# Performance work log

Measured on AMD Instinct MI355X. Metric: run time of the kernel, lower is better.

The kernel has to match this reference:

```python
import jax, jax.numpy as jnp
import numpy as np

NUM_HEADS = 16
NUM_KV_HEADS = 4
HEAD_DIM = 128
ROPE_BASE = 10000.0


def _apply_rope(x):
    # x: [B, H, S, D], interleaved RoPE: x1 = x[..., ::2], x2 = x[..., 1::2]
    B, H, S, D = x.shape
    inv_freq = 1.0 / (ROPE_BASE ** (jnp.arange(0, D, 2, dtype=jnp.float32) / D))  # [D/2]
    t = jnp.arange(S, dtype=jnp.float32)
    freqs = t[:, None] * inv_freq[None, :]          # [S, D/2]
    cos = jnp.cos(freqs)[None, None]                # [1,1,S,D/2]
    sin = jnp.sin(freqs)[None, None]
    xr = x.reshape(B, H, S, D // 2, 2)
    x1, x2 = xr[..., 0], xr[..., 1]
    r1 = x1 * cos - x2 * sin
    r2 = x1 * sin + x2 * cos
    return jnp.stack([r1, r2], axis=-1).reshape(B, H, S, D)


def setup_inputs() -> dict:
    key = jax.random.key(0)
    ks = jax.random.split(key, 5)
    H = NUM_HEADS * HEAD_DIM          # 2048
    KV = NUM_KV_HEADS * HEAD_DIM      # 512
    std = 0.02
    return {
        "hidden_states": jax.random.normal(ks[0], (1, 4096, H), dtype=jnp.float32),
        "wq": jax.random.normal(ks[1], (H, H), dtype=jnp.float32) * std,
        "wk": jax.random.normal(ks[2], (H, KV), dtype=jnp.float32) * std,
        "wv": jax.random.normal(ks[3], (H, KV), dtype=jnp.float32) * std,
        "wo": jax.random.normal(ks[4], (H, H), dtype=jnp.float32) * std,
    }


def reference(hidden_states, wq, wk, wv, wo):
    B, S, H = hidden_states.shape
    nh, nkv, hd = NUM_HEADS, NUM_KV_HEADS, HEAD_DIM
    scale = 1.0 / np.sqrt(hd)

    q = (hidden_states @ wq).reshape(B, S, nh, hd).transpose(0, 2, 1, 3)   # [B,nh,S,hd]
    k = (hidden_states @ wk).reshape(B, S, nkv, hd).transpose(0, 2, 1, 3)  # [B,nkv,S,hd]
    v = (hidden_states @ wv).reshape(B, S, nkv, hd).transpose(0, 2, 1, 3)

    q = _apply_rope(q)
    k = _apply_rope(k)

    rep = nh // nkv
    k = jnp.repeat(k, rep, axis=1)  # GQA head repetition -> [B,nh,S,hd]
    v = jnp.repeat(v, rep, axis=1)

    scores = jnp.einsum("bhqd,bhkd->bhqk", q, k) * scale
    causal = jnp.tril(jnp.ones((S, S), dtype=bool))
    scores = jnp.where(causal[None, None], scores, jnp.float32(-1e30))
    probs = jax.nn.softmax(scores, axis=-1)
    attn = jnp.einsum("bhqk,bhkd->bhqd", probs, v)      # [B,nh,S,hd]
    attn = attn.transpose(0, 2, 1, 3).reshape(B, S, H)
    return attn @ wo
```

## Files before the change

kernel.cpp:

```cpp
#include <hip/hip_runtime.h>

typedef unsigned short u16;
typedef unsigned int u32;
typedef __bf16 bf16x8 __attribute__((ext_vector_type(8)));
typedef float f32x4 __attribute__((ext_vector_type(4)));
typedef float f32x16 __attribute__((ext_vector_type(16)));
typedef int v2i __attribute__((ext_vector_type(2)));

#define S_LEN 4096
#define HDIM 2048
#define KVDIM 512
#define N_HEADS 16
#define HEAD_D 128

__device__ __forceinline__ u16 f2bf(float f) {
  u32 u = __float_as_uint(f);
  u32 r = (u + 0x7FFFu + ((u >> 16) & 1u)) >> 16;
  return (u16)r;
}
__device__ __forceinline__ float bf2f(u16 h) {
  return __uint_as_float(((u32)h) << 16);
}
__device__ __forceinline__ float exp2_fast(float x) {
  float r;
  asm("v_exp_f32 %0, %1" : "=v"(r) : "v"(x));
  return r;
}
__device__ __forceinline__ u32 cvt_pk_bf16(float lo, float hi) {
  u32 r;
  asm("v_cvt_pk_bf16_f32 %0, %1, %2" : "=v"(r) : "v"(lo), "v"(hi));
  return r;
}
__device__ __forceinline__ void gload16(const u16* g, const u16* l) {
  __builtin_amdgcn_global_load_lds(
      (const __attribute__((address_space(1))) void*)g,
      (__attribute__((address_space(3))) void*)l, 16, 0, 0);
}

__global__ void k_prep(const float* __restrict__ in, u16* __restrict__ out,
                       float* __restrict__ cosT, float* __restrict__ sinT) {
  int b = blockIdx.x;
  int tid = threadIdx.x;
  if (b < 4096) {
    int i = b * 256 + tid;
    const float4* p = reinterpret_cast<const float4*>(in) + (size_t)i * 2;
    float4 a = p[0], c = p[1];
    u32 o0 = (u32)f2bf(a.x) | ((u32)f2bf(a.y) << 16);
    u32 o1 = (u32)f2bf(a.z) | ((u32)f2bf(a.w) << 16);
    u32 o2 = (u32)f2bf(c.x) | ((u32)f2bf(c.y) << 16);
    u32 o3 = (u32)f2bf(c.z) | ((u32)f2bf(c.w) << 16);
    reinterpret_cast<uint4*>(out)[i] = make_uint4(o0, o1, o2, o3);
  } else {
    int i = (b - 4096) * 256 + tid;
    int pos = i >> 6, f = i & 63;
    float inv = expf(-0.1439115683121279f * (float)f);
    float ang = (float)pos * inv;
    float s, c;
    sincosf(ang, &s, &c);
    cosT[i] = c;
    sinT[i] = s;
  }
}

__global__ void k_transpose_all(const float* __restrict__ wq, const float* __restrict__ wk,
                                const float* __restrict__ wv, const float* __restrict__ wo,
                                u16* __restrict__ WqT, u16* __restrict__ WkT,
                                u16* __restrict__ WvT, u16* __restrict__ WoT) {
  __shared__ float t[32][33];
  int b = blockIdx.x;
  const float* W;
  u16* Wt;
  int Kd, Nd, bx, by;
  if (b < 4096) {
    W = wq; Wt = WqT; Kd = HDIM; Nd = HDIM; bx = b & 63; by = b >> 6;
  } else if (b < 5120) {
    int r = b - 4096; W = wk; Wt = WkT; Kd = HDIM; Nd = KVDIM; bx = r & 15; by = r >> 4;
  } else if (b < 6144) {
    int r = b - 5120; W = wv; Wt = WvT; Kd = HDIM; Nd = KVDIM; bx = r & 15; by = r >> 4;
  } else {
    int r = b - 6144; W = wo; Wt = WoT; Kd = HDIM; Nd = HDIM; bx = r & 63; by = r >> 6;
  }
  int tx = threadIdx.x & 31, ty = threadIdx.x >> 5;
  int n = bx * 32 + tx;
  for (int j = ty; j < 32; j += 8)
    t[j][tx] = W[(size_t)(by * 32 + j) * Nd + n];
  __syncthreads();
  int k = by * 32 + tx;
  for (int j = ty; j < 32; j += 8)
    Wt[(size_t)(bx * 32 + j) * Kd + k] = f2bf(t[tx][j]);
}

__global__ void k_rope_all(u16* __restrict__ Qb, u16* __restrict__ Kb,
                           const float* __restrict__ cosT, const float* __restrict__ sinT) {
  int b = blockIdx.x;
  u16* X;
  int width, i;
  if (b < 4096) { X = Qb; width = HDIM; i = b * 256 + threadIdx.x; }
  else { X = Kb; width = KVDIM; i = (b - 4096) * 256 + threadIdx.x; }
  size_t idx = (size_t)i * 8;
  int row = (int)(idx / width);
  int col = (int)(idx - (size_t)row * width);
  int fi = (col & 127) >> 1;
  float4 c4 = *reinterpret_cast<const float4*>(&cosT[(row << 6) + fi]);
  float4 s4 = *reinterpret_cast<const float4*>(&sinT[(row << 6) + fi]);
  uint4 v = *reinterpret_cast<const uint4*>(&X[idx]);
  float cc[4] = {c4.x, c4.y, c4.z, c4.w};
  float ss[4] = {s4.x, s4.y, s4.z, s4.w};
  u32 w_[4] = {v.x, v.y, v.z, v.w};
  u32 r_[4];
#pragma unroll
  for (int p = 0; p < 4; ++p) {
    float x1 = bf2f((u16)(w_[p] & 0xffff));
    float x2 = bf2f((u16)(w_[p] >> 16));
    float r1 = x1 * cc[p] - x2 * ss[p];
    float r2 = x1 * ss[p] + x2 * cc[p];
    r_[p] = (u32)f2bf(r1) | ((u32)f2bf(r2) << 16);
  }
  *reinterpret_cast<uint4*>(&X[idx]) = make_uint4(r_[0], r_[1], r_[2], r_[3]);
}

__global__ __launch_bounds__(256) void k_gemm_qkv(
    const u16* __restrict__ A, const u16* __restrict__ WqT, const u16* __restrict__ WkT,
    const u16* __restrict__ WvT, u16* __restrict__ Qb, u16* __restrict__ Kb,
    u16* __restrict__ VTb) {
  const int Kd = HDIM, M = S_LEN;
  __shared__ __align__(16) u16 As[128 * 32];
  __shared__ __align__(16) u16 Bs[128 * 32];
  const int p = blockIdx.x;
  const int bmg = p & 7, r = p >> 3;
  const int bm = (bmg * 4 + (r & 3)) * 128;
  const int by = r >> 2;
  const u16* Bt;
  int bn, N, mode;
  if (by < 16) { Bt = WqT; bn = by * 128; N = HDIM; mode = 0; }
  else if (by < 20) { Bt = WkT; bn = (by - 16) * 128; N = KVDIM; mode = 1; }
  else { Bt = WvT; bn = (by - 20) * 128; N = KVDIM; mode = 2; }
  const int tid = threadIdx.x;
  const int lane = tid & 63;
  const int wid = tid >> 6;
  const int wr = (wid >> 1) * 64, wc = (wid & 1) * 64;
  const int lr = lane & 15, lhi = lane >> 4;
  const int srow = lane >> 2;
  const int skc = (lane & 3) * 8;
  f32x4 acc[4][4] = {};
  for (int k0 = 0; k0 < Kd; k0 += 32) {
#pragma unroll
    for (int it = 0; it < 2; ++it) {
      int rowbase = (it * 4 + wid) * 16;
      gload16(&A[(size_t)(bm + rowbase + srow) * Kd + k0 + skc], &As[rowbase * 32]);
      gload16(&Bt[(size_t)(bn + rowbase + srow) * Kd + k0 + skc], &Bs[rowbase * 32]);
    }
    __syncthreads();
    bf16x8 af[4], bfr[4];
#pragma unroll
    for (int m = 0; m < 4; ++m)
      af[m] = *reinterpret_cast<const bf16x8*>(&As[(wr + m * 16 + lr) * 32 + lhi * 8]);
#pragma unroll
    for (int n = 0; n < 4; ++n)
      bfr[n] = *reinterpret_cast<const bf16x8*>(&Bs[(wc + n * 16 + lr) * 32 + lhi * 8]);
#pragma unroll
    for (int m = 0; m < 4; ++m)
#pragma unroll
      for (int n = 0; n < 4; ++n)
        acc[m][n] = __builtin_amdgcn_mfma_f32_16x16x32_bf16(af[m], bfr[n], acc[m][n], 0, 0, 0);
    __syncthreads();
  }
#pragma unroll
  for (int m = 0; m < 4; ++m) {
    int grow0 = bm + wr + m * 16 + lhi * 4;
#pragma unroll
    for (int n = 0; n < 4; ++n) {
      int gcol = bn + wc + n * 16 + lr;
      if (mode == 2) {
        ushort4 pk;
        pk.x = f2bf(acc[m][n][0]);
        pk.y = f2bf(acc[m][n][1]);
        pk.z = f2bf(acc[m][n][2]);
        pk.w = f2bf(acc[m][n][3]);
        *reinterpret_cast<ushort4*>(&VTb[(size_t)gcol * M + grow0]) = pk;
      } else {
        u16* outp = (mode == 0) ? Qb : Kb;
#pragma unroll
        for (int r2 = 0; r2 < 4; ++r2)
          outp[(size_t)(grow0 + r2) * N + gcol] = f2bf(acc[m][n][r2]);
      }
    }
  }
}

__global__ __launch_bounds__(256) void k_gemm_bt(
    const u16* __restrict__ A, const u16* __restrict__ Bt, float* __restrict__ Cout,
    int M, int N, int Kd) {
  __shared__ __align__(16) u16 As[128 * 32];
  __shared__ __align__(16) u16 Bs[128 * 32];
  const int p = blockIdx.x;
  const int bmg = p & 7, r = p >> 3;
  const int bm = (bmg * 4 + (r & 3)) * 128;
  const int bn = (r >> 2) * 128;
  const int tid = threadIdx.x;
  const int lane = tid & 63;
  const int wid = tid >> 6;
  const int wr = (wid >> 1) * 64, wc = (wid & 1) * 64;
  const int lr = lane & 15, lhi = lane >> 4;
  const int srow = lane >> 2;
  const int skc = (lane & 3) * 8;
  f32x4 acc[4][4] = {};
  for (int k0 = 0; k0 < Kd; k0 += 32) {
#pragma unroll
    for (int it = 0; it < 2; ++it) {
      int rowbase = (it * 4 + wid) * 16;
      gload16(&A[(size_t)(bm + rowbase + srow) * Kd + k0 + skc], &As[rowbase * 32]);
      gload16(&Bt[(size_t)(bn + rowbase + srow) * Kd + k0 + skc], &Bs[rowbase * 32]);
    }
    __syncthreads();
    bf16x8 af[4], bfr[4];
#pragma unroll
    for (int m = 0; m < 4; ++m)
      af[m] = *reinterpret_cast<const bf16x8*>(&As[(wr + m * 16 + lr) * 32 + lhi * 8]);
#pragma unroll
    for (int n = 0; n < 4; ++n)
      bfr[n] = *reinterpret_cast<const bf16x8*>(&Bs[(wc + n * 16 + lr) * 32 + lhi * 8]);
#pragma unroll
    for (int m = 0; m < 4; ++m)
#pragma unroll
      for (int n = 0; n < 4; ++n)
        acc[m][n] = __builtin_amdgcn_mfma_f32_16x16x32_bf16(af[m], bfr[n], acc[m][n], 0, 0, 0);
    __syncthreads();
  }
#pragma unroll
  for (int m = 0; m < 4; ++m) {
    int grow0 = bm + wr + m * 16 + lhi * 4;
#pragma unroll
    for (int n = 0; n < 4; ++n) {
      int gcol = bn + wc + n * 16 + lr;
#pragma unroll
      for (int r2 = 0; r2 < 4; ++r2)
        Cout[(size_t)(grow0 + r2) * N + gcol] = acc[m][n][r2];
    }
  }
}

__global__ __launch_bounds__(256, 2) void k_attn(
    const u16* __restrict__ Q, const u16* __restrict__ K, const u16* __restrict__ VT,
    u16* __restrict__ PO0, u16* __restrict__ PO1, float2* __restrict__ ML) {
  __shared__ __align__(16) u16 Ks[64 * 128];
  __shared__ __align__(16) u16 Vs[128 * 64];
  int i = blockIdx.x;
  const int kvhalf = i >> 9;
  int jj = i & 511;
  int qt, h;
  if (jj < 256) { qt = 16 + (jj & 15); h = jj >> 4; }
  else { int j2 = jj - 256; qt = 15 - (j2 & 15); h = j2 >> 4; }
  const int kvh = h >> 2;
  const int tid = threadIdx.x, lane = tid & 63, wid = tid >> 6;
  const int l31 = lane & 31, hi = lane >> 5;
  const int qw = qt * 128 + wid * 32;
  const int qglob = qw + l31;
  const float CE = 0.12751743f;
  const float THR = 62.74f;

  const u16* qptr = &Q[(size_t)qglob * HDIM + h * HEAD_D];
  bf16x8 qf[8];
#pragma unroll
  for (int ks = 0; ks < 8; ++ks)
    qf[ks] = *reinterpret_cast<const bf16x8*>(&qptr[ks * 16 + hi * 8]);

  f32x16 o_[4] = {};
  float m_ = -3e38f, l_ = 0.f;
  char* KsB = (char*)Ks;
  char* VsB = (char*)Vs;

  const int j0 = kvhalf * (qt + 1);
  const int j1 = j0 + qt + 1;
  for (int j = j0; j < j1; ++j) {
    const int kb = j << 6;
    __syncthreads();
#pragma unroll
    for (int it = 0; it < 4; ++it) {
      int s = it * 256 + tid;
      int kv = s >> 4, c16 = s & 15;
      int db = kv * 256 + c16 * 16;
      db ^= ((db >> 8) & 7) << 4;
      *reinterpret_cast<uint4*>(KsB + db) = *reinterpret_cast<const uint4*>(
          &K[(size_t)(kb + kv) * KVDIM + kvh * HEAD_D + c16 * 8]);
    }
#pragma unroll
    for (int it = 0; it < 4; ++it) {
      int s = it * 256 + tid;
      int d = s >> 3, k16 = s & 7;
      int db = d * 128 + k16 * 16;
      db ^= ((db >> 7) & 7) << 4;
      *reinterpret_cast<uint4*>(VsB + db) = *reinterpret_cast<const uint4*>(
          &VT[(size_t)(kvh * HEAD_D + d) * S_LEN + kb + k16 * 8]);
    }
    __syncthreads();

    if (kb <= qw + 31) {
      f32x16 s0 = {}, s1 = {};
#pragma unroll
      for (int ks = 0; ks < 8; ++ks) {
        int db0 = l31 * 256 + ks * 32 + hi * 16;
        db0 ^= ((db0 >> 8) & 7) << 4;
        int db1 = (32 + l31) * 256 + ks * 32 + hi * 16;
        db1 ^= ((db1 >> 8) & 7) << 4;
        bf16x8 k0 = *reinterpret_cast<const bf16x8*>(KsB + db0);
        bf16x8 k1 = *reinterpret_cast<const bf16x8*>(KsB + db1);
        s0 = __builtin_amdgcn_mfma_f32_32x32x16_bf16(k0, qf[ks], s0, 0, 0, 0);
        s1 = __builtin_amdgcn_mfma_f32_32x32x16_bf16(k1, qf[ks], s1, 0, 0, 0);
      }
      if (kb + 63 > qw) {
#pragma unroll
        for (int r = 0; r < 16; ++r) {
          int kvr = kb + (r & 3) + 8 * (r >> 2) + 4 * hi;
          if (kvr > qglob) s0[r] = -1e30f;
          if (kvr + 32 > qglob) s1[r] = -1e30f;
        }
      }
      float pm = fmaxf(s0[0], s1[0]);
#pragma unroll
      for (int r = 1; r < 16; ++r) pm = fmaxf(pm, fmaxf(s0[r], s1[r]));
      pm = fmaxf(pm, __shfl_xor(pm, 32));
      if (!__all(pm <= m_ + THR)) {
        float mnew = fmaxf(m_, pm);
        float fac = exp2_fast((m_ - mnew) * CE);
        m_ = mnew;
        l_ *= fac;
#pragma unroll
        for (int dt = 0; dt < 4; ++dt)
#pragma unroll
          for (int r = 0; r < 16; ++r) o_[dt][r] *= fac;
      }
      const float mc = m_ * CE;
      float rs = 0.f;
#pragma unroll
      for (int r = 0; r < 16; ++r) {
        s0[r] = exp2_fast(__builtin_fmaf(s0[r], CE, -mc));
        s1[r] = exp2_fast(__builtin_fmaf(s1[r], CE, -mc));
        rs += s0[r] + s1[r];
      }
      rs += __shfl_xor(rs, 32);
      l_ += rs;
#pragma unroll
      for (int kvt = 0; kvt < 2; ++kvt) {
        u32 xw[8], yw[8];
#pragma unroll
        for (int g = 0; g < 8; ++g) {
          float plo = kvt ? s1[2 * g] : s0[2 * g];
          float phi = kvt ? s1[2 * g + 1] : s0[2 * g + 1];
          u32 pw = cvt_pk_bf16(plo, phi);
          v2i sw = __builtin_amdgcn_permlane32_swap((int)pw, (int)pw, false, false);
          xw[g] = (u32)sw[0];
          yw[g] = (u32)sw[1];
        }
#pragma unroll
        for (int ksl = 0; ksl < 2; ++ksl) {
          int b = ksl * 4;
          u32 f0 = hi ? xw[b + 2] : xw[b + 0];
          u32 f1 = hi ? xw[b + 3] : xw[b + 1];
          u32 f2 = hi ? yw[b + 2] : yw[b + 0];
          u32 f3 = hi ? yw[b + 3] : yw[b + 1];
          uint4 fr = make_uint4(f0, f1, f2, f3);
          bf16x8 pf = *reinterpret_cast<bf16x8*>(&fr);
          const int kvstep = kvt * 2 + ksl;
#pragma unroll
          for (int dt = 0; dt < 4; ++dt) {
            int db = (dt * 32 + l31) * 128 + kvstep * 32 + hi * 16;
            db ^= ((db >> 7) & 7) << 4;
            bf16x8 vf = *reinterpret_cast<const bf16x8*>(VsB + db);
            o_[dt] = __builtin_amdgcn_mfma_f32_32x32x16_bf16(vf, pf, o_[dt], 0, 0, 0);
          }
        }
      }
    }
  }
  const float inv_l = (l_ > 0.f) ? (1.0f / l_) : 0.f;
  u16* PO = kvhalf ? PO1 : PO0;
  u16* optr = &PO[(size_t)qglob * HDIM + h * HEAD_D];
#pragma unroll
  for (int dt = 0; dt < 4; ++dt)
#pragma unroll
    for (int g = 0; g < 4; ++g) {
      ushort4 pk;
      pk.x = f2bf(o_[dt][4 * g + 0] * inv_l);
      pk.y = f2bf(o_[dt][4 * g + 1] * inv_l);
      pk.z = f2bf(o_[dt][4 * g + 2] * inv_l);
      pk.w = f2bf(o_[dt][4 * g + 3] * inv_l);
      *reinterpret_cast<ushort4*>(&optr[dt * 32 + g * 8 + hi * 4]) = pk;
    }
  if (hi == 0)
    ML[(size_t)kvhalf * N_HEADS * S_LEN + (size_t)h * S_LEN + qglob] =
        make_float2(m_, l_);
}

__global__ void k_combine(const u16* __restrict__ PO0, const u16* __restrict__ PO1,
                          const float2* __restrict__ ML, u16* __restrict__ Out) {
  int i = blockIdx.x * 256 + threadIdx.x;
  int d8 = (i & 15) * 8;
  int qh = i >> 4;
  int h = qh & 15, q = qh >> 4;
  const float CE = 0.12751743f;
  float2 ml1 = ML[(size_t)h * S_LEN + q];
  float2 ml2 = ML[(size_t)N_HEADS * S_LEN + (size_t)h * S_LEN + q];
  float m = fmaxf(ml1.x, ml2.x);
  float w1 = ml1.y * exp2_fast((ml1.x - m) * CE);
  float w2 = ml2.y * exp2_fast((ml2.x - m) * CE);
  float inv = 1.0f / (w1 + w2);
  w1 *= inv;
  w2 *= inv;
  size_t base = (size_t)q * HDIM + h * HEAD_D + d8;
  uint4 a = *reinterpret_cast<const uint4*>(&PO0[base]);
  uint4 b = *reinterpret_cast<const uint4*>(&PO1[base]);
  u32 aw[4] = {a.x, a.y, a.z, a.w}, bw[4] = {b.x, b.y, b.z, b.w};
  u32 ow[4];
#pragma unroll
  for (int p = 0; p < 4; ++p) {
    float lo = w1 * bf2f((u16)(aw[p] & 0xffff)) + w2 * bf2f((u16)(bw[p] & 0xffff));
    float hi2 = w1 * bf2f((u16)(aw[p] >> 16)) + w2 * bf2f((u16)(bw[p] >> 16));
    ow[p] = (u32)f2bf(lo) | ((u32)f2bf(hi2) << 16);
  }
  *reinterpret_cast<uint4*>(&Out[base]) = make_uint4(ow[0], ow[1], ow[2], ow[3]);
}

extern "C" void kernel_launch(void* const* d_in, const int* in_sizes, int n_in,
                              void* d_out, int out_size, void* d_ws, size_t ws_size,
                              hipStream_t stream) {
  const float* hs = (const float*)d_in[0];
  const float* wq = (const float*)d_in[1];
  const float* wk = (const float*)d_in[2];
  const float* wv = (const float*)d_in[3];
  const float* wo = (const float*)d_in[4];

  char* ws = (char*)d_ws;
  size_t off = 0;
  auto alloc = [&](size_t bytes) {
    void* p = ws + off;
    off += (bytes + 255) & ~(size_t)255;
    return p;
  };
  u16* Xb = (u16*)alloc((size_t)S_LEN * HDIM * 2);
  u16* WqT = (u16*)alloc((size_t)HDIM * HDIM * 2);
  u16* WkT = (u16*)alloc((size_t)KVDIM * HDIM * 2);
  u16* WvT = (u16*)alloc((size_t)KVDIM * HDIM * 2);
  u16* WoT = (u16*)alloc((size_t)HDIM * HDIM * 2);
  u16* Qb = (u16*)alloc((size_t)S_LEN * HDIM * 2);
  u16* Kb = (u16*)alloc((size_t)S_LEN * KVDIM * 2);
  u16* VTb = (u16*)alloc((size_t)KVDIM * S_LEN * 2);
  u16* Ab = (u16*)alloc((size_t)S_LEN * HDIM * 2);
  float* cosT = (float*)alloc((size_t)S_LEN * 64 * 4);
  float* sinT = (float*)alloc((size_t)S_LEN * 64 * 4);
  if (off > ws_size) return;

  u16* PO0 = Ab;
  u16* PO1 = Xb;
  float2* ML = (float2*)WqT;

  k_prep<<<dim3(5120), dim3(256), 0, stream>>>(hs, Xb, cosT, sinT);
  k_transpose_all<<<dim3(10240), dim3(256), 0, stream>>>(wq, wk, wv, wo, WqT, WkT, WvT, WoT);
  k_gemm_qkv<<<dim3(768), dim3(256), 0, stream>>>(Xb, WqT, WkT, WvT, Qb, Kb, VTb);
  k_rope_all<<<dim3(5120), dim3(256), 0, stream>>>(Qb, Kb, cosT, sinT);
  k_attn<<<dim3(1024), dim3(256), 0, stream>>>(Qb, Kb, VTb, PO0, PO1, ML);
  k_combine<<<dim3(4096), dim3(256), 0, stream>>>(PO0, PO1, ML, Ab);
  k_gemm_bt<<<dim3(512), dim3(256), 0, stream>>>(Ab, WoT, (float*)d_out, S_LEN, HDIM, HDIM);
}
```

Before: 277.4 us.

## Fuse RoPE into QKV epilogue, combine into output GEMM, merge prep kernels

The input conversion, cos/sin table generation and weight transposes now share one launch instead of two. RoPE is applied in the QKV GEMM epilogue: each lane swaps its value with its neighbour via __shfl_xor and combines it with cos/sin read from the tables. The split-KV combine is folded into the output GEMM's A-tile load, so the pass that read the two partial outputs and wrote a merged buffer goes away. The cost is that the output GEMM now does synchronous global loads plus combine arithmetic, replacing the async global_load_lds, and repeats that work for every N tile.

```diff
diff --git a/kernel.cpp b/kernel.cpp
--- a/kernel.cpp
+++ b/kernel.cpp
@@ -37,8 +37,13 @@
       (__attribute__((address_space(3))) void*)l, 16, 0, 0);
 }
 
-__global__ void k_prep(const float* __restrict__ in, u16* __restrict__ out,
-                       float* __restrict__ cosT, float* __restrict__ sinT) {
+__global__ void k_prep_all(const float* __restrict__ in, u16* __restrict__ out,
+                           float* __restrict__ cosT, float* __restrict__ sinT,
+                           const float* __restrict__ wq, const float* __restrict__ wk,
+                           const float* __restrict__ wv, const float* __restrict__ wo,
+                           u16* __restrict__ WqT, u16* __restrict__ WkT,
+                           u16* __restrict__ WvT, u16* __restrict__ WoT) {
+  __shared__ float t[32][33];
   int b = blockIdx.x;
   int tid = threadIdx.x;
   if (b < 4096) {
@@ -50,7 +55,9 @@
     u32 o2 = (u32)f2bf(c.x) | ((u32)f2bf(c.y) << 16);
     u32 o3 = (u32)f2bf(c.z) | ((u32)f2bf(c.w) << 16);
     reinterpret_cast<uint4*>(out)[i] = make_uint4(o0, o1, o2, o3);
-  } else {
+    return;
+  }
+  if (b < 5120) {
     int i = (b - 4096) * 256 + tid;
     int pos = i >> 6, f = i & 63;
     float inv = expf(-0.1439115683121279f * (float)f);
@@ -59,28 +66,22 @@
     sincosf(ang, &s, &c);
     cosT[i] = c;
     sinT[i] = s;
-  }
-}
-
-__global__ void k_transpose_all(const float* __restrict__ wq, const float* __restrict__ wk,
-                                const float* __restrict__ wv, const float* __restrict__ wo,
-                                u16* __restrict__ WqT, u16* __restrict__ WkT,
-                                u16* __restrict__ WvT, u16* __restrict__ WoT) {
-  __shared__ float t[32][33];
-  int b = blockIdx.x;
+    return;
+  }
+  int bb = b - 5120;
   const float* W;
   u16* Wt;
   int Kd, Nd, bx, by;
-  if (b < 4096) {
-    W = wq; Wt = WqT; Kd = HDIM; Nd = HDIM; bx = b & 63; by = b >> 6;
-  } else if (b < 5120) {
-    int r = b - 4096; W = wk; Wt = WkT; Kd = HDIM; Nd = KVDIM; bx = r & 15; by = r >> 4;
-  } else if (b < 6144) {
-    int r = b - 5120; W = wv; Wt = WvT; Kd = HDIM; Nd = KVDIM; bx = r & 15; by = r >> 4;
+  if (bb < 4096) {
+    W = wq; Wt = WqT; Kd = HDIM; Nd = HDIM; bx = bb & 63; by = bb >> 6;
+  } else if (bb < 5120) {
+    int r = bb - 4096; W = wk; Wt = WkT; Kd = HDIM; Nd = KVDIM; bx = r & 15; by = r >> 4;
+  } else if (bb < 6144) {
+    int r = bb - 5120; W = wv; Wt = WvT; Kd = HDIM; Nd = KVDIM; bx = r & 15; by = r >> 4;
   } else {
-    int r = b - 6144; W = wo; Wt = WoT; Kd = HDIM; Nd = HDIM; bx = r & 63; by = r >> 6;
-  }
-  int tx = threadIdx.x & 31, ty = threadIdx.x >> 5;
+    int r = bb - 6144; W = wo; Wt = WoT; Kd = HDIM; Nd = HDIM; bx = r & 63; by = r >> 6;
+  }
+  int tx = tid & 31, ty = tid >> 5;
   int n = bx * 32 + tx;
   for (int j = ty; j < 32; j += 8)
     t[j][tx] = W[(size_t)(by * 32 + j) * Nd + n];
@@ -90,38 +91,10 @@
     Wt[(size_t)(bx * 32 + j) * Kd + k] = f2bf(t[tx][j]);
 }
 
-__global__ void k_rope_all(u16* __restrict__ Qb, u16* __restrict__ Kb,
-                           const float* __restrict__ cosT, const float* __restrict__ sinT) {
-  int b = blockIdx.x;
-  u16* X;
-  int width, i;
-  if (b < 4096) { X = Qb; width = HDIM; i = b * 256 + threadIdx.x; }
-  else { X = Kb; width = KVDIM; i = (b - 4096) * 256 + threadIdx.x; }
-  size_t idx = (size_t)i * 8;
-  int row = (int)(idx / width);
-  int col = (int)(idx - (size_t)row * width);
-  int fi = (col & 127) >> 1;
-  float4 c4 = *reinterpret_cast<const float4*>(&cosT[(row << 6) + fi]);
-  float4 s4 = *reinterpret_cast<const float4*>(&sinT[(row << 6) + fi]);
-  uint4 v = *reinterpret_cast<const uint4*>(&X[idx]);
-  float cc[4] = {c4.x, c4.y, c4.z, c4.w};
-  float ss[4] = {s4.x, s4.y, s4.z, s4.w};
-  u32 w_[4] = {v.x, v.y, v.z, v.w};
-  u32 r_[4];
-#pragma unroll
-  for (int p = 0; p < 4; ++p) {
-    float x1 = bf2f((u16)(w_[p] & 0xffff));
-    float x2 = bf2f((u16)(w_[p] >> 16));
-    float r1 = x1 * cc[p] - x2 * ss[p];
-    float r2 = x1 * ss[p] + x2 * cc[p];
-    r_[p] = (u32)f2bf(r1) | ((u32)f2bf(r2) << 16);
-  }
-  *reinterpret_cast<uint4*>(&X[idx]) = make_uint4(r_[0], r_[1], r_[2], r_[3]);
-}
-
 __global__ __launch_bounds__(256) void k_gemm_qkv(
     const u16* __restrict__ A, const u16* __restrict__ WqT, const u16* __restrict__ WkT,
-    const u16* __restrict__ WvT, u16* __restrict__ Qb, u16* __restrict__ Kb,
+    const u16* __restrict__ WvT, const float* __restrict__ cosT,
+    const float* __restrict__ sinT, u16* __restrict__ Qb, u16* __restrict__ Kb,
     u16* __restrict__ VTb) {
   const int Kd = HDIM, M = S_LEN;
   __shared__ __align__(16) u16 As[128 * 32];
@@ -165,6 +138,7 @@
         acc[m][n] = __builtin_amdgcn_mfma_f32_16x16x32_bf16(af[m], bfr[n], acc[m][n], 0, 0, 0);
     __syncthreads();
   }
+  const float odd_sign = (lr & 1) ? 1.0f : -1.0f;
 #pragma unroll
   for (int m = 0; m < 4; ++m) {
     int grow0 = bm + wr + m * 16 + lhi * 4;
@@ -180,17 +154,27 @@
         *reinterpret_cast<ushort4*>(&VTb[(size_t)gcol * M + grow0]) = pk;
       } else {
         u16* outp = (mode == 0) ? Qb : Kb;
-#pragma unroll
-        for (int r2 = 0; r2 < 4; ++r2)
-          outp[(size_t)(grow0 + r2) * N + gcol] = f2bf(acc[m][n][r2]);
+        const int fi = (gcol & 127) >> 1;
+#pragma unroll
+        for (int r2 = 0; r2 < 4; ++r2) {
+          float v = acc[m][n][r2];
+          float pv = __shfl_xor(v, 1);
+          int pos = grow0 + r2;
+          float c = cosT[(pos << 6) + fi];
+          float s = sinT[(pos << 6) + fi];
+          float res = __builtin_fmaf(pv, odd_sign * s, v * c);
+          outp[(size_t)pos * N + gcol] = f2bf(res);
+        }
       }
     }
   }
 }
 
 __global__ __launch_bounds__(256) void k_gemm_bt(
-    const u16* __restrict__ A, const u16* __restrict__ Bt, float* __restrict__ Cout,
-    int M, int N, int Kd) {
+    const u16* __restrict__ PO0, const u16* __restrict__ PO1,
+    const float2* __restrict__ ML, const u16* __restrict__ Bt,
+    float* __restrict__ Cout) {
+  const int M = S_LEN, N = HDIM, Kd = HDIM;
   __shared__ __align__(16) u16 As[128 * 32];
   __shared__ __align__(16) u16 Bs[128 * 32];
   const int p = blockIdx.x;
@@ -204,12 +188,35 @@
   const int lr = lane & 15, lhi = lane >> 4;
   const int srow = lane >> 2;
   const int skc = (lane & 3) * 8;
+  const float CE = 0.12751743f;
   f32x4 acc[4][4] = {};
   for (int k0 = 0; k0 < Kd; k0 += 32) {
+    const int hh = (k0 + skc) >> 7;
 #pragma unroll
     for (int it = 0; it < 2; ++it) {
       int rowbase = (it * 4 + wid) * 16;
-      gload16(&A[(size_t)(bm + rowbase + srow) * Kd + k0 + skc], &As[rowbase * 32]);
+      int row = bm + rowbase + srow;
+      float2 ml1 = ML[(size_t)hh * S_LEN + row];
+      float2 ml2 = ML[(size_t)N_HEADS * S_LEN + (size_t)hh * S_LEN + row];
+      float mm = fmaxf(ml1.x, ml2.x);
+      float w1 = ml1.y * exp2_fast((ml1.x - mm) * CE);
+      float w2 = ml2.y * exp2_fast((ml2.x - mm) * CE);
+      float inv = 1.0f / (w1 + w2);
+      w1 *= inv;
+      w2 *= inv;
+      size_t gbase = (size_t)row * Kd + k0 + skc;
+      uint4 a = *reinterpret_cast<const uint4*>(&PO0[gbase]);
+      uint4 b = *reinterpret_cast<const uint4*>(&PO1[gbase]);
+      u32 aw[4] = {a.x, a.y, a.z, a.w}, bw[4] = {b.x, b.y, b.z, b.w};
+      u32 ow[4];
+#pragma unroll
+      for (int q = 0; q < 4; ++q) {
+        float lo = w1 * bf2f((u16)(aw[q] & 0xffff)) + w2 * bf2f((u16)(bw[q] & 0xffff));
+        float hi2 = w1 * bf2f((u16)(aw[q] >> 16)) + w2 * bf2f((u16)(bw[q] >> 16));
+        ow[q] = cvt_pk_bf16(lo, hi2);
+      }
+      *reinterpret_cast<uint4*>(&As[(rowbase + srow) * 32 + skc]) =
+          make_uint4(ow[0], ow[1], ow[2], ow[3]);
       gload16(&Bt[(size_t)(bn + rowbase + srow) * Kd + k0 + skc], &Bs[rowbase * 32]);
     }
     __syncthreads();
@@ -390,35 +397,6 @@
   if (hi == 0)
     ML[(size_t)kvhalf * N_HEADS * S_LEN + (size_t)h * S_LEN + qglob] =
         make_float2(m_, l_);
-}
-
-__global__ void k_combine(const u16* __restrict__ PO0, const u16* __restrict__ PO1,
-                          const float2* __restrict__ ML, u16* __restrict__ Out) {
-  int i = blockIdx.x * 256 + threadIdx.x;
-  int d8 = (i & 15) * 8;
-  int qh = i >> 4;
-  int h = qh & 15, q = qh >> 4;
-  const float CE = 0.12751743f;
-  float2 ml1 = ML[(size_t)h * S_LEN + q];
-  float2 ml2 = ML[(size_t)N_HEADS * S_LEN + (size_t)h * S_LEN + q];
-  float m = fmaxf(ml1.x, ml2.x);
-  float w1 = ml1.y * exp2_fast((ml1.x - m) * CE);
-  float w2 = ml2.y * exp2_fast((ml2.x - m) * CE);
-  float inv = 1.0f / (w1 + w2);
-  w1 *= inv;
-  w2 *= inv;
-  size_t base = (size_t)q * HDIM + h * HEAD_D + d8;
-  uint4 a = *reinterpret_cast<const uint4*>(&PO0[base]);
-  uint4 b = *reinterpret_cast<const uint4*>(&PO1[base]);
-  u32 aw[4] = {a.x, a.y, a.z, a.w}, bw[4] = {b.x, b.y, b.z, b.w};
-  u32 ow[4];
-#pragma unroll
-  for (int p = 0; p < 4; ++p) {
-    float lo = w1 * bf2f((u16)(aw[p] & 0xffff)) + w2 * bf2f((u16)(bw[p] & 0xffff));
-    float hi2 = w1 * bf2f((u16)(aw[p] >> 16)) + w2 * bf2f((u16)(bw[p] >> 16));
-    ow[p] = (u32)f2bf(lo) | ((u32)f2bf(hi2) << 16);
-  }
-  *reinterpret_cast<uint4*>(&Out[base]) = make_uint4(ow[0], ow[1], ow[2], ow[3]);
 }
 
 extern "C" void kernel_launch(void* const* d_in, const int* in_sizes, int n_in,
@@ -454,11 +432,9 @@
   u16* PO1 = Xb;
   float2* ML = (float2*)WqT;
 
-  k_prep<<<dim3(5120), dim3(256), 0, stream>>>(hs, Xb, cosT, sinT);
-  k_transpose_all<<<dim3(10240), dim3(256), 0, stream>>>(wq, wk, wv, wo, WqT, WkT, WvT, WoT);
-  k_gemm_qkv<<<dim3(768), dim3(256), 0, stream>>>(Xb, WqT, WkT, WvT, Qb, Kb, VTb);
-  k_rope_all<<<dim3(5120), dim3(256), 0, stream>>>(Qb, Kb, cosT, sinT);
+  k_prep_all<<<dim3(15360), dim3(256), 0, stream>>>(hs, Xb, cosT, sinT, wq, wk, wv, wo,
+                                                    WqT, WkT, WvT, WoT);
+  k_gemm_qkv<<<dim3(768), dim3(256), 0, stream>>>(Xb, WqT, WkT, WvT, cosT, sinT, Qb, Kb, VTb);
   k_attn<<<dim3(1024), dim3(256), 0, stream>>>(Qb, Kb, VTb, PO0, PO1, ML);
-  k_combine<<<dim3(4096), dim3(256), 0, stream>>>(PO0, PO1, ML, Ab);
-  k_gemm_bt<<<dim3(512), dim3(256), 0, stream>>>(Ab, WoT, (float*)d_out, S_LEN, HDIM, HDIM);
-}
+  k_gemm_bt<<<dim3(512), dim3(256), 0, stream>>>(PO0, PO1, ML, WoT, (float*)d_out);
+}
```

Result: slower. 313.9 us (+13.1%).
